# Optimization experiments

Hardware: AMD Instinct MI355X
Metric: run time of the kernel (lower is better)

The kernel has to match this reference:

```python
import jax, jax.numpy as jnp
import numpy as np


def _sobel_kernels(dtype):
    # Faithful to the torch code: each kernel has shape (1,3,3) in (kd,kh,kw),
    # i.e. a 2D Sobel applied slice-wise, but conv3d uses padding=1 on ALL dims
    # so the output depth is D+2.
    sx = np.array([[[-1, 0, 1], [-2, 0, 2], [-1, 0, 1]]], dtype=np.float32)  # (1,3,3)
    sy = np.transpose(sx, (0, 2, 1))                                          # transpose(1,2)
    sz = np.array([[[-1, -2, -1], [0, 0, 0], [1, 2, 1]]], dtype=np.float32)
    k = np.stack([sx, sy, sz])[:, None]  # (3 out, 1 in, 1, 3, 3)
    return jnp.asarray(k, dtype)


def setup_inputs() -> dict:
    key = jax.random.key(0)
    k1, k2 = jax.random.split(key)
    B, C, D, H, W = 2, 4, 96, 160, 160
    pred = jax.random.normal(k1, (B, C, D, H, W), dtype=jnp.float32)
    target = jax.random.randint(k2, (B, D, H, W), 0, C)
    return {"pred": pred, "target": target}


def reference(pred, target):
    B, C, D, H, W = pred.shape
    p = jax.nn.softmax(pred, axis=1)                                   # (B,C,D,H,W)
    t = jax.nn.one_hot(target, C, dtype=pred.dtype)                    # (B,D,H,W,C)
    t = jnp.transpose(t, (0, 4, 1, 2, 3))                              # (B,C,D,H,W)
    k = _sobel_kernels(pred.dtype)

    def sobel(x):
        # fold class into batch; 3 output channels = x/y/z gradients
        x = x.reshape(B * C, 1, D, H, W)
        return jax.lax.conv_general_dilated(
            x, k, window_strides=(1, 1, 1), padding=[(1, 1)] * 3,
            dimension_numbers=("NCDHW", "OIDHW", "NCDHW"))           # (B*C,3,D+2,H+2,W+2)

    diff = sobel(p) - sobel(t)
    # Each torch mse_loss averages over a (B,1,D+2,H+2,W+2) tensor; the 3*C
    # means are summed, then divided by num_classes.
    per_tensor = B * (D + 2) * (H + 2) * (W + 2)
    loss = jnp.sum(diff * diff) / per_tensor / C
    return loss
```

## Files before the change

### kernel.cpp

```cpp
#include <hip/hip_runtime.h>

#define NB 2
#define NC 4
#define ND 96
#define NH 160
#define NW 160

constexpr int TW = 80, TH = 32;
constexpr int SW = TW + 2, SH = TH + 2;
constexpr int NTW = NW / TW;
constexpr int NTH = NH / TH;
constexpr int TILES = NTW * NTH;

constexpr float SCALE = 1.0f / (2.0f * 98.0f * 162.0f * 162.0f * 4.0f);

__global__ __launch_bounds__(256) void boundary_loss_kernel(
    const float* __restrict__ pred,
    const int*   __restrict__ target,
    float* __restrict__ out)
{
    __shared__ float q[NC][SH * SW];

    const int tid   = threadIdx.x;
    const int slice = blockIdx.y;
    const int b     = slice / ND;
    const int d     = slice - b * ND;
    const int tile  = blockIdx.x;
    const int th0   = (tile / NTW) * TH;
    const int tw0   = (tile % NTW) * TW;

    const size_t cstride   = (size_t)ND * NH * NW;
    const size_t sliceBase = ((size_t)b * NC * ND + d) * (NH * NW);
    const size_t tgtBase   = ((size_t)b * ND + d) * (NH * NW);

    for (int idx = tid; idx < SH * SW; idx += 256) {
        const int r  = idx / SW;
        const int cc = idx - r * SW;
        const int gh = th0 + r - 1;
        const int gw = tw0 + cc - 1;
        float q0 = 0.f, q1 = 0.f, q2 = 0.f, q3 = 0.f;
        if (gh >= 0 && gh < NH && gw >= 0 && gw < NW) {
            const size_t off = sliceBase + (size_t)gh * NW + gw;
            const float p0 = pred[off];
            const float p1 = pred[off + cstride];
            const float p2 = pred[off + 2 * cstride];
            const float p3 = pred[off + 3 * cstride];
            const int   t  = target[tgtBase + (size_t)gh * NW + gw];
            const float m  = fmaxf(fmaxf(p0, p1), fmaxf(p2, p3));
            const float e0 = __expf(p0 - m);
            const float e1 = __expf(p1 - m);
            const float e2 = __expf(p2 - m);
            const float e3 = __expf(p3 - m);
            const float inv = 1.0f / (e0 + e1 + e2 + e3);
            q0 = e0 * inv - (t == 0 ? 1.0f : 0.0f);
            q1 = e1 * inv - (t == 1 ? 1.0f : 0.0f);
            q2 = e2 * inv - (t == 2 ? 1.0f : 0.0f);
            q3 = e3 * inv - (t == 3 ? 1.0f : 0.0f);
        }
        q[0][idx] = q0;
        q[1][idx] = q1;
        q[2][idx] = q2;
        q[3][idx] = q3;
    }
    __syncthreads();

    float acc = 0.f;
    #pragma unroll
    for (int i = 0; i < (TW * TH) / 256; ++i) {
        const int pid = tid + i * 256;
        const int r   = pid / TW + 1;
        const int cc  = pid - (r - 1) * TW + 1;
        #pragma unroll
        for (int c = 0; c < NC; ++c) {
            const float* s = q[c];
            const float a00 = s[(r - 1) * SW + cc - 1];
            const float a01 = s[(r - 1) * SW + cc];
            const float a02 = s[(r - 1) * SW + cc + 1];
            const float a10 = s[r * SW + cc - 1];
            const float a12 = s[r * SW + cc + 1];
            const float a20 = s[(r + 1) * SW + cc - 1];
            const float a21 = s[(r + 1) * SW + cc];
            const float a22 = s[(r + 1) * SW + cc + 1];
            const float gx = (a02 - a00) + 2.f * (a12 - a10) + (a22 - a20);
            const float gy = (a20 - a00) + 2.f * (a21 - a01) + (a22 - a02);
            acc += gx * gx + 2.f * gy * gy;
        }
    }

    #pragma unroll
    for (int off = 32; off > 0; off >>= 1)
        acc += __shfl_down(acc, off, 64);
    __shared__ float wsum[4];
    if ((tid & 63) == 0) wsum[tid >> 6] = acc;
    __syncthreads();
    if (tid == 0) {
        const float s = wsum[0] + wsum[1] + wsum[2] + wsum[3];
        atomicAdd(out, s * SCALE);
    }
}

extern "C" void kernel_launch(void* const* d_in, const int* in_sizes, int n_in,
                              void* d_out, int out_size, void* d_ws, size_t ws_size,
                              hipStream_t stream) {
    const float* pred   = (const float*)d_in[0];
    const int*   target = (const int*)d_in[1];
    float*       out    = (float*)d_out;

    hipMemsetAsync(out, 0, sizeof(float), stream);

    dim3 grid(TILES, NB * ND);
    boundary_loss_kernel<<<grid, 256, 0, stream>>>(pred, target, out);
}
```

Measured before the change: 154.9 us.

## Replace shared-memory tiles with per-wavefront register row streaming and lane shuffles

Each wavefront now handles a 62-column strip over 20 rows and slides down them. Horizontal neighbours come from lane shuffles, and the vertical Sobel sums sit in rolling registers, so the LDS tile and block barriers are gone. Each wave atomically adds its partial sum directly, and the reciprocal uses a fast rcp intrinsic. In exchange, halo rows are recomputed per chunk, two of 64 lanes per wave are wasted at strip edges, and there are many more atomics on one address.

```diff
diff --git a/kernel.cpp b/kernel.cpp
--- a/kernel.cpp
+++ b/kernel.cpp
@@ -6,12 +6,11 @@
 #define NH 160
 #define NW 160
 
-constexpr int TW = 80, TH = 32;
-constexpr int SW = TW + 2, SH = TH + 2;
-constexpr int NTW = NW / TW;
-constexpr int NTH = NH / TH;
-constexpr int TILES = NTW * NTH;
-
+constexpr int R      = 20;
+constexpr int NCHUNK = NH / R;
+constexpr int NSTRIP = 3;
+constexpr int NSLICE = NB * ND;
+constexpr int NTASK  = NSLICE * NSTRIP * NCHUNK;
 constexpr float SCALE = 1.0f / (2.0f * 98.0f * 162.0f * 162.0f * 4.0f);
 
 __global__ __launch_bounds__(256) void boundary_loss_kernel(
@@ -19,84 +18,76 @@
     const int*   __restrict__ target,
     float* __restrict__ out)
 {
-    __shared__ float q[NC][SH * SW];
+    const int wid  = blockIdx.x * 4 + (threadIdx.x >> 6);
+    const int lane = threadIdx.x & 63;
 
-    const int tid   = threadIdx.x;
-    const int slice = blockIdx.y;
+    const int chunk = wid % NCHUNK;
+    const int tmp   = wid / NCHUNK;
+    const int strip = tmp % NSTRIP;
+    const int slice = tmp / NSTRIP;
     const int b     = slice / ND;
     const int d     = slice - b * ND;
-    const int tile  = blockIdx.x;
-    const int th0   = (tile / NTW) * TH;
-    const int tw0   = (tile % NTW) * TW;
 
-    const size_t cstride   = (size_t)ND * NH * NW;
-    const size_t sliceBase = ((size_t)b * NC * ND + d) * (NH * NW);
-    const size_t tgtBase   = ((size_t)b * ND + d) * (NH * NW);
+    const int  x    = strip * 62 + lane - 1;
+    const bool colv = (x >= 0) && (x < NW);
+    const bool outm = (lane >= 1) && (lane <= 62) && (x < NW);
+    const int  y0   = chunk * R;
 
-    for (int idx = tid; idx < SH * SW; idx += 256) {
-        const int r  = idx / SW;
-        const int cc = idx - r * SW;
-        const int gh = th0 + r - 1;
-        const int gw = tw0 + cc - 1;
+    const size_t cs    = (size_t)ND * NH * NW;
+    const size_t pbase = ((size_t)b * NC * ND + d) * (size_t)(NH * NW);
+    const size_t tbase = ((size_t)b * ND + d) * (size_t)(NH * NW);
+
+    float smm[NC], sm[NC], dmm[NC], dm[NC];
+    #pragma unroll
+    for (int c = 0; c < NC; ++c) { smm[c] = sm[c] = dmm[c] = dm[c] = 0.f; }
+
+    float acc = 0.f;
+
+    for (int t = 0; t < R + 2; ++t) {
+        const int gy = y0 - 1 + t;
         float q0 = 0.f, q1 = 0.f, q2 = 0.f, q3 = 0.f;
-        if (gh >= 0 && gh < NH && gw >= 0 && gw < NW) {
-            const size_t off = sliceBase + (size_t)gh * NW + gw;
+        if (colv && gy >= 0 && gy < NH) {
+            const size_t off = pbase + (size_t)gy * NW + x;
             const float p0 = pred[off];
-            const float p1 = pred[off + cstride];
-            const float p2 = pred[off + 2 * cstride];
-            const float p3 = pred[off + 3 * cstride];
-            const int   t  = target[tgtBase + (size_t)gh * NW + gw];
+            const float p1 = pred[off + cs];
+            const float p2 = pred[off + 2 * cs];
+            const float p3 = pred[off + 3 * cs];
+            const int   tg = target[tbase + (size_t)gy * NW + x];
             const float m  = fmaxf(fmaxf(p0, p1), fmaxf(p2, p3));
             const float e0 = __expf(p0 - m);
             const float e1 = __expf(p1 - m);
             const float e2 = __expf(p2 - m);
             const float e3 = __expf(p3 - m);
-            const float inv = 1.0f / (e0 + e1 + e2 + e3);
-            q0 = e0 * inv - (t == 0 ? 1.0f : 0.0f);
-            q1 = e1 * inv - (t == 1 ? 1.0f : 0.0f);
-            q2 = e2 * inv - (t == 2 ? 1.0f : 0.0f);
-            q3 = e3 * inv - (t == 3 ? 1.0f : 0.0f);
+            const float inv = __builtin_amdgcn_rcpf(e0 + e1 + e2 + e3);
+            q0 = e0 * inv - (tg == 0 ? 1.f : 0.f);
+            q1 = e1 * inv - (tg == 1 ? 1.f : 0.f);
+            q2 = e2 * inv - (tg == 2 ? 1.f : 0.f);
+            q3 = e3 * inv - (tg == 3 ? 1.f : 0.f);
         }
-        q[0][idx] = q0;
-        q[1][idx] = q1;
-        q[2][idx] = q2;
-        q[3][idx] = q3;
-    }
-    __syncthreads();
+        float q[NC] = {q0, q1, q2, q3};
 
-    float acc = 0.f;
-    #pragma unroll
-    for (int i = 0; i < (TW * TH) / 256; ++i) {
-        const int pid = tid + i * 256;
-        const int r   = pid / TW + 1;
-        const int cc  = pid - (r - 1) * TW + 1;
+        float rowacc = 0.f;
         #pragma unroll
         for (int c = 0; c < NC; ++c) {
-            const float* s = q[c];
-            const float a00 = s[(r - 1) * SW + cc - 1];
-            const float a01 = s[(r - 1) * SW + cc];
-            const float a02 = s[(r - 1) * SW + cc + 1];
-            const float a10 = s[r * SW + cc - 1];
-            const float a12 = s[r * SW + cc + 1];
-            const float a20 = s[(r + 1) * SW + cc - 1];
-            const float a21 = s[(r + 1) * SW + cc];
-            const float a22 = s[(r + 1) * SW + cc + 1];
-            const float gx = (a02 - a00) + 2.f * (a12 - a10) + (a22 - a20);
-            const float gy = (a20 - a00) + 2.f * (a21 - a01) + (a22 - a02);
-            acc += gx * gx + 2.f * gy * gy;
+            const float ql = __shfl_up(q[c], 1, 64);
+            const float qr = __shfl_down(q[c], 1, 64);
+            const float sn = ql + 2.f * q[c] + qr;
+            const float dn = qr - ql;
+            if (t >= 2) {
+                const float gx  = dmm[c] + 2.f * dm[c] + dn;
+                const float gyv = sn - smm[c];
+                rowacc += gx * gx + 2.f * gyv * gyv;
+            }
+            smm[c] = sm[c]; sm[c] = sn;
+            dmm[c] = dm[c]; dm[c] = dn;
         }
+        if (t >= 2 && outm) acc += rowacc;
     }
 
     #pragma unroll
     for (int off = 32; off > 0; off >>= 1)
         acc += __shfl_down(acc, off, 64);
-    __shared__ float wsum[4];
-    if ((tid & 63) == 0) wsum[tid >> 6] = acc;
-    __syncthreads();
-    if (tid == 0) {
-        const float s = wsum[0] + wsum[1] + wsum[2] + wsum[3];
-        atomicAdd(out, s * SCALE);
-    }
+    if (lane == 0) atomicAdd(out, acc * SCALE);
 }
 
 extern "C" void kernel_launch(void* const* d_in, const int* in_sizes, int n_in,
@@ -108,6 +99,5 @@
 
     hipMemsetAsync(out, 0, sizeof(float), stream);
 
-    dim3 grid(TILES, NB * ND);
-    boundary_loss_kernel<<<grid, 256, 0, stream>>>(pred, target, out);
+    boundary_loss_kernel<<<NTASK / 4, 256, 0, stream>>>(pred, target, out);
 }
```

New measurement: 183.7 us. 1.19x slower.
